# Performance work log

Hardware: AMD Instinct MI355X
Metric: run time of the kernel (lower is better)

## Reference

```python
import jax, jax.numpy as jnp
import numpy as np

B = 8            # graphs per batch
NP = 1000        # nodes per graph (fixed 1000x1000 connectivity)
N = B * NP       # total nodes
F = 1000         # node feature dim (== NP)
HC = 32          # hidden_channels
NL = 3           # num_layers (HC*NL == 96, the hard-coded bnh dim)
K = 5            # Chebyshev order
HID = 128        # mlp hidden
NC = 2           # num_classes
DEG = 10         # avg degree
E = N * DEG      # total edges
TRI = F * (F - 1) // 2   # 499500 strict-upper-triangle entries
EPS = 1e-5


def setup_inputs():
    ks = jax.random.split(jax.random.key(0), 16)
    x = jax.random.normal(ks[0], (N, F), jnp.float32)  # per-graph connectivity rows
    # block-structured edges: endpoints stay inside their own graph
    offs = jnp.repeat(jnp.arange(B, dtype=jnp.int32) * NP, NP * DEG)
    src = jax.random.randint(ks[1], (E,), 0, NP, jnp.int32) + offs
    dst = jax.random.randint(ks[2], (E,), 0, NP, jnp.int32) + offs
    edge_index = jnp.stack([src, dst])
    batch = jnp.repeat(jnp.arange(B, dtype=jnp.int32), NP)
    nrm = lambda k, shape, s=0.05: jax.random.normal(k, shape, jnp.float32) * s
    return dict(
        x=x, edge_index=edge_index, batch=batch,
        conv_w0=nrm(ks[3], (K, F, HC)), conv_b0=jnp.zeros((HC,), jnp.float32),
        conv_w1=nrm(ks[4], (K, HC, HC)), conv_b1=jnp.zeros((HC,), jnp.float32),
        conv_w2=nrm(ks[5], (K, HC, HC)), conv_b2=jnp.zeros((HC,), jnp.float32),
        bnh_g=jnp.ones((HC * NL,), jnp.float32), bnh_b=jnp.zeros((HC * NL,), jnp.float32),
        bn_g=jnp.ones((TRI,), jnp.float32), bn_b=jnp.zeros((TRI,), jnp.float32),
        mlp_w1=nrm(ks[6], (TRI, HID), 0.002), mlp_b1=jnp.zeros((HID,), jnp.float32),
        bn1_g=jnp.ones((HID,), jnp.float32), bn1_b=jnp.zeros((HID,), jnp.float32),
        mlp_w2=nrm(ks[7], (HID, HID // 2)), mlp_b2=jnp.zeros((HID // 2,), jnp.float32),
        bn2_g=jnp.ones((HID // 2,), jnp.float32), bn2_b=jnp.zeros((HID // 2,), jnp.float32),
        mlp_w3=nrm(ks[8], (HID // 2, HID // 2)), mlp_b3=jnp.zeros((HID // 2,), jnp.float32),
        bn3_g=jnp.ones((HID // 2,), jnp.float32), bn3_b=jnp.zeros((HID // 2,), jnp.float32),
        mlp_w4=nrm(ks[9], (HID // 2, NC)), mlp_b4=jnp.zeros((NC,), jnp.float32),
    )


def _bn(z, g, b):
    # BatchNorm1d in training mode (batch stats, biased var), eps=1e-5
    m = jnp.mean(z, axis=0)
    v = jnp.var(z, axis=0)
    return (z - m) * jax.lax.rsqrt(v + EPS) * g + b


def _cheb(z, src, dst, w, Ws, b):
    # PyG ChebConv with sym norm, lambda_max=2: L~ = -D^{-1/2} A D^{-1/2}
    prop = lambda t: jax.ops.segment_sum(w[:, None] * t[src], dst, num_segments=N)
    Tx0, out = z, z @ Ws[0]
    Tx1 = prop(z)
    out = out + Tx1 @ Ws[1]
    for k in range(2, Ws.shape[0]):
        Tx2 = 2.0 * prop(Tx1) - Tx0
        out = out + Tx2 @ Ws[k]
        Tx0, Tx1 = Tx1, Tx2
    return out + b


def reference(x, edge_index, batch, conv_w0, conv_b0, conv_w1, conv_b1, conv_w2, conv_b2,
              bnh_g, bnh_b, bn_g, bn_b, mlp_w1, mlp_b1, bn1_g, bn1_b,
              mlp_w2, mlp_b2, bn2_g, bn2_b, mlp_w3, mlp_b3, bn3_g, bn3_b, mlp_w4, mlp_b4):
    src, dst = edge_index[0], edge_index[1]
    # symmetric normalization weights (negated scaled Laplacian off-diagonal)
    deg = jax.ops.segment_sum(jnp.ones((E,), x.dtype), src, num_segments=N)
    dinv = jnp.where(deg > 0, deg ** -0.5, 0.0)
    w = -dinv[src] * dinv[dst]
    # node features replaced by tiled identity, as in the original forward
    xid = jnp.tile(jnp.eye(NP, dtype=x.dtype), (B, 1))  # [N, F]
    h1 = jnp.tanh(_cheb(xid, src, dst, w, conv_w0, conv_b0))
    h2 = jnp.tanh(_cheb(h1, src, dst, w, conv_w1, conv_b1))
    h3 = jnp.tanh(_cheb(h2, src, dst, w, conv_w2, conv_b2))
    # MeanAggregation per graph
    cnt = jax.ops.segment_sum(jnp.ones((N,), x.dtype), batch, num_segments=B)[:, None]
    pool = lambda h: jax.ops.segment_sum(h, batch, num_segments=B) / cnt
    emb = jnp.concatenate([pool(h1), pool(h2), pool(h3)], axis=1)  # [B, 96]
    hbn = _bn(emb, bnh_g, bnh_b)
    # static strict-upper-triangle gather (replaces per-graph triu().nonzero())
    rawx = x.reshape(B, F, F)
    iu0, iu1 = np.triu_indices(F, k=1)
    feats = rawx[:, iu0, iu1]                       # [B, 499500]
    fbn = _bn(feats, bn_g, bn_b)
    # MLP (dropout = identity / eval)
    a = jax.nn.relu(_bn(fbn @ mlp_w1 + mlp_b1, bn1_g, bn1_b))
    a = jax.nn.relu(_bn(a @ mlp_w2 + mlp_b2, bn2_g, bn2_b))
    a = jax.nn.relu(_bn(a @ mlp_w3 + mlp_b3, bn3_g, bn3_b))
    logits = a @ mlp_w4 + mlp_b4
    logp = jax.nn.log_softmax(logits, axis=1)
    return logp, hbn
```

## Files before the change

### kernel.cpp

```cpp
#include <hip/hip_runtime.h>

#define NN 8000
#define NPP 1000
#define FF 1000
#define HCC 32
#define KK 5
#define EE 80000
#define TRIN 499500
#define HID 128
#define EPSV 1e-5f
#define NREP 64

#define IDX_ACC  0
#define IDX_DEGI 65536
#define IDX_CNT  73536
#define IDX_FILL 81536
#define ZERO_N   89536
#define IDX_ROWS 89600
#define IDX_EPAK 97664
#define IDX_H1   257664
#define IDX_H2   513664
#define IDX_EMB  769664


__global__ void k_count(const int* __restrict__ src, const int* __restrict__ dst,
                        int* __restrict__ degi, int* __restrict__ cnt) {
  int e = blockIdx.x * blockDim.x + threadIdx.x;
  if (e >= EE) return;
  atomicAdd(&degi[src[e]], 1);
  atomicAdd(&cnt[dst[e]], 1);
}

__global__ void k_scan(const int* __restrict__ cnt, int* __restrict__ rows) {
  __shared__ int ssum[1024];
  int tid = threadIdx.x;
  int base = tid * 8;
  int loc[8];
  int s = 0;
#pragma unroll
  for (int q = 0; q < 8; ++q) {
    int idx = base + q;
    int v = (idx < NN) ? cnt[idx] : 0;
    loc[q] = s;
    s += v;
  }
  ssum[tid] = s;
  __syncthreads();
  for (int d = 1; d < 1024; d <<= 1) {
    int v = (tid >= d) ? ssum[tid - d] : 0;
    __syncthreads();
    ssum[tid] += v;
    __syncthreads();
  }
  int off = (tid == 0) ? 0 : ssum[tid - 1];
#pragma unroll
  for (int q = 0; q < 8; ++q) {
    int idx = base + q;
    if (idx < NN) rows[idx] = off + loc[q];
  }
  if (tid == 1023) rows[NN] = EE;
}

__global__ void k_fill(const int* __restrict__ src, const int* __restrict__ dst,
                       const int* __restrict__ degi, const int* __restrict__ rows,
                       int* __restrict__ fill, int2* __restrict__ epak) {
  int e = blockIdx.x * blockDim.x + threadIdx.x;
  if (e >= EE) return;
  int s = src[e], d = dst[e];
  int pos = rows[d] + atomicAdd(&fill[d], 1);
  int dd = degi[d];
  float w = -rsqrtf((float)degi[s]) * ((dd > 0) ? rsqrtf((float)dd) : 0.0f);
  int2 pk;
  pk.x = s % NPP;
  pk.y = __float_as_int(w);
  epak[pos] = pk;
}

__global__ void __launch_bounds__(1024, 4) k_layer(
    const float* __restrict__ cw, const float* __restrict__ bias,
    const float* __restrict__ hin, float* __restrict__ hout,
    const int* __restrict__ rows, const int2* __restrict__ epak,
    float* __restrict__ emb, int L) {
  __shared__ float ckl[KK][NPP];
  __shared__ float bcur[NPP];
  __shared__ float wcol[KK][HCC];
  __shared__ float part[32];
  const int t = threadIdx.x;
  const int g = blockIdx.x >> 5;
  const int c = blockIdx.x & 31;
  const bool act = t < NPP;
  if (hin == nullptr) {
    if (act) {
#pragma unroll
      for (int k = 0; k < KK; ++k)
        ckl[k][t] = cw[k * (FF * HCC) + t * HCC + c];
    }
  } else {
    if (t < KK * HCC) {
      int k = t >> 5, j = t & 31;
      wcol[k][j] = cw[k * (HCC * HCC) + j * HCC + c];
    }
    __syncthreads();
    if (act) {
      float hrow[HCC];
      const float* hp = hin + ((size_t)g * NPP + t) * HCC;
#pragma unroll
      for (int q = 0; q < HCC / 4; ++q) {
        float4 f = *(const float4*)(hp + q * 4);
        hrow[q * 4 + 0] = f.x; hrow[q * 4 + 1] = f.y;
        hrow[q * 4 + 2] = f.z; hrow[q * 4 + 3] = f.w;
      }
#pragma unroll
      for (int k = 0; k < KK; ++k) {
        float a = 0.0f;
#pragma unroll
        for (int j = 0; j < HCC; ++j) a += hrow[j] * wcol[k][j];
        ckl[k][t] = a;
      }
    }
  }
  __syncthreads();
  int r0 = 0, r1 = 0;
  if (act) {
    bcur[t] = ckl[4][t];
    r0 = rows[g * NPP + t];
    r1 = rows[g * NPP + t + 1];
  }
  float bprev = 0.0f;
  float v = 0.0f;
  __syncthreads();
#pragma unroll
  for (int step = 0; step < 4; ++step) {
    const float alpha = (step == 3) ? 1.0f : 2.0f;
    const int kidx = 3 - step;
    if (act) {
      float acc = 0.0f;
      for (int e = r0; e < r1; ++e) {
        int2 pk = epak[e];
        acc += __int_as_float(pk.y) * bcur[pk.x];
      }
      v = alpha * acc - bprev + ckl[kidx][t];
    }
    __syncthreads();
    if (act) {
      bprev = bcur[t];
      bcur[t] = v;
    }
    __syncthreads();
  }
  if (act) {
    float h = tanhf(v + bias[c]);
    if (hout) hout[((size_t)g * NPP + t) * HCC + c] = h;
    bcur[t] = h;
  }
  __syncthreads();
  if (t < 32) {
    float s = 0.0f;
    for (int i = t; i < NPP; i += 32) s += bcur[i];
    part[t] = s;
  }
  __syncthreads();
  if (t == 0) {
    float s = 0.0f;
#pragma unroll
    for (int q = 0; q < 32; ++q) s += part[q];
    emb[g * 96 + L * HCC + c] = s * (1.0f / (float)NPP);
  }
}


__device__ __forceinline__ int tri_S(int i) { return i * 999 - (i * (i - 1)) / 2; }

__global__ void __launch_bounds__(256) k_gemm1(const float* __restrict__ x,
                                               const float* __restrict__ bng,
                                               const float* __restrict__ bnb,
                                               const float* __restrict__ W1,
                                               float* __restrict__ accrep) {
  __shared__ float fbn_s[256][8];
  __shared__ float red[8][128];
  const int tid = threadIdx.x;
  const int c4 = (tid & 31) * 4;
  const int stripe = tid >> 5;
  const int j0 = blockIdx.x * 256;
  float acc[8][4];
#pragma unroll
  for (int b = 0; b < 8; ++b)
#pragma unroll
    for (int q = 0; q < 4; ++q) acc[b][q] = 0.0f;

  {
    const int j = j0 + tid;
    float vals[8];
    if (j < TRIN) {
      const float tt = 1999.0f;
      int i = (int)((tt - sqrtf(tt * tt - 8.0f * (float)j)) * 0.5f);
      i = max(0, min(i, 998));
      while (tri_S(i + 1) <= j) ++i;
      while (tri_S(i) > j) --i;
      int i1 = j - tri_S(i) + i + 1;
      size_t base = (size_t)i * FF + i1;
#pragma unroll
      for (int b = 0; b < 8; ++b) vals[b] = x[(size_t)b * (FF * NPP) + base];
      float m = 0.0f;
#pragma unroll
      for (int b = 0; b < 8; ++b) m += vals[b];
      m *= 0.125f;
      float va = 0.0f;
#pragma unroll
      for (int b = 0; b < 8; ++b) { float d = vals[b] - m; va += d * d; }
      va *= 0.125f;
      float sc = bng[j] * rsqrtf(va + EPSV);
      float tb = bnb[j] - m * sc;
#pragma unroll
      for (int b = 0; b < 8; ++b) vals[b] = sc * vals[b] + tb;
    } else {
#pragma unroll
      for (int b = 0; b < 8; ++b) vals[b] = 0.0f;
    }
    *(float4*)&fbn_s[tid][0] = make_float4(vals[0], vals[1], vals[2], vals[3]);
    *(float4*)&fbn_s[tid][4] = make_float4(vals[4], vals[5], vals[6], vals[7]);
  }
  __syncthreads();

  const int jbase = stripe * 32;
  const int jmax = min(32, TRIN - j0 - jbase);
  const float* wp = W1 + (size_t)(j0 + jbase) * HID + c4;
  if (jmax == 32) {
#pragma unroll 4
    for (int jj = 0; jj < 32; ++jj) {
      float4 w = *(const float4*)(wp + (size_t)jj * HID);
      float4 f0 = *(const float4*)&fbn_s[jbase + jj][0];
      float4 f1 = *(const float4*)&fbn_s[jbase + jj][4];
      float wv[4] = {w.x, w.y, w.z, w.w};
      float fv[8] = {f0.x, f0.y, f0.z, f0.w, f1.x, f1.y, f1.z, f1.w};
#pragma unroll
      for (int b = 0; b < 8; ++b)
#pragma unroll
        for (int q = 0; q < 4; ++q) acc[b][q] += fv[b] * wv[q];
    }
  } else {
    for (int jj = 0; jj < jmax; ++jj) {
      float4 w = *(const float4*)(wp + (size_t)jj * HID);
      float4 f0 = *(const float4*)&fbn_s[jbase + jj][0];
      float4 f1 = *(const float4*)&fbn_s[jbase + jj][4];
      float wv[4] = {w.x, w.y, w.z, w.w};
      float fv[8] = {f0.x, f0.y, f0.z, f0.w, f1.x, f1.y, f1.z, f1.w};
#pragma unroll
      for (int b = 0; b < 8; ++b)
#pragma unroll
        for (int q = 0; q < 4; ++q) acc[b][q] += fv[b] * wv[q];
    }
  }
#pragma unroll
  for (int b = 0; b < 8; ++b) {
    __syncthreads();
    red[stripe][c4 + 0] = acc[b][0];
    red[stripe][c4 + 1] = acc[b][1];
    red[stripe][c4 + 2] = acc[b][2];
    red[stripe][c4 + 3] = acc[b][3];
    __syncthreads();
    if (tid < 128) {
      float s = 0.0f;
#pragma unroll
      for (int q = 0; q < 8; ++q) s += red[q][tid];
      atomicAdd(&accrep[(blockIdx.x & (NREP - 1)) * 1024 + b * HID + tid], s);
    }
  }
}


__global__ void __launch_bounds__(1024) k_mlp(
    const float* __restrict__ accrep, const float* __restrict__ emb,
    const float* __restrict__ hg, const float* __restrict__ hb,
    const float* __restrict__ mb1,
    const float* __restrict__ g1, const float* __restrict__ be1,
    const float* __restrict__ W2, const float* __restrict__ mb2,
    const float* __restrict__ g2, const float* __restrict__ be2,
    const float* __restrict__ W3, const float* __restrict__ mb3,
    const float* __restrict__ g3, const float* __restrict__ be3,
    const float* __restrict__ W4, const float* __restrict__ mb4,
    float* __restrict__ out) {
  __shared__ float A[8][128];
  __shared__ float V[8][128];
  __shared__ float Bm[8][64];
  __shared__ float Cm[8][64];
  __shared__ float lg[8][2];
  const int tid = threadIdx.x;
  if (tid < 96) {
    float v[8];
    float m = 0.0f;
#pragma unroll
    for (int q = 0; q < 8; ++q) { v[q] = emb[q * 96 + tid]; m += v[q]; }
    m *= 0.125f;
    float va = 0.0f;
#pragma unroll
    for (int q = 0; q < 8; ++q) { float d = v[q] - m; va += d * d; }
    va *= 0.125f;
    float s = hg[tid] * rsqrtf(va + EPSV);
    float t = hb[tid] - m * s;
#pragma unroll
    for (int q = 0; q < 8; ++q) out[16 + q * 96 + tid] = s * v[q] + t;
  }
  {
    const int c = tid & 127;
    const int b = tid >> 7;
    float a = mb1[c];
    for (int rep = 0; rep < NREP; ++rep) a += accrep[rep * 1024 + tid];
    V[b][c] = a;
  }
  __syncthreads();
  {
    const int c = tid & 127;
    const int b = tid >> 7;
    float m = 0.0f;
#pragma unroll
    for (int q = 0; q < 8; ++q) m += V[q][c];
    m *= 0.125f;
    float va = 0.0f;
#pragma unroll
    for (int q = 0; q < 8; ++q) { float d = V[q][c] - m; va += d * d; }
    va *= 0.125f;
    float s = g1[c] * rsqrtf(va + EPSV);
    float t = be1[c] - m * s;
    float z = s * V[b][c] + t;
    A[b][c] = (z > 0.0f) ? z : 0.0f;
  }
  __syncthreads();
  if (tid < 512) {
    const int c = tid & 63;
    const int b = tid >> 6;
    float a = mb2[c];
    for (int j = 0; j < 128; ++j) a += A[b][j] * W2[j * 64 + c];
    V[b][c] = a;
  }
  __syncthreads();
  if (tid < 512) {
    const int c = tid & 63;
    const int b = tid >> 6;
    float m = 0.0f;
#pragma unroll
    for (int q = 0; q < 8; ++q) m += V[q][c];
    m *= 0.125f;
    float va = 0.0f;
#pragma unroll
    for (int q = 0; q < 8; ++q) { float d = V[q][c] - m; va += d * d; }
    va *= 0.125f;
    float s = g2[c] * rsqrtf(va + EPSV);
    float t = be2[c] - m * s;
    float z = s * V[b][c] + t;
    Bm[b][c] = (z > 0.0f) ? z : 0.0f;
  }
  __syncthreads();
  if (tid < 512) {
    const int c = tid & 63;
    const int b = tid >> 6;
    float a = mb3[c];
    for (int j = 0; j < 64; ++j) a += Bm[b][j] * W3[j * 64 + c];
    V[b][c] = a;
  }
  __syncthreads();
  if (tid < 512) {
    const int c = tid & 63;
    const int b = tid >> 6;
    float m = 0.0f;
#pragma unroll
    for (int q = 0; q < 8; ++q) m += V[q][c];
    m *= 0.125f;
    float va = 0.0f;
#pragma unroll
    for (int q = 0; q < 8; ++q) { float d = V[q][c] - m; va += d * d; }
    va *= 0.125f;
    float s = g3[c] * rsqrtf(va + EPSV);
    float t = be3[c] - m * s;
    float z = s * V[b][c] + t;
    Cm[b][c] = (z > 0.0f) ? z : 0.0f;
  }
  __syncthreads();
  if (tid < 16) {
    int b = tid >> 1, c = tid & 1;
    float a4 = mb4[c];
    for (int j = 0; j < 64; ++j) a4 += Cm[b][j] * W4[j * 2 + c];
    lg[b][c] = a4;
  }
  __syncthreads();
  if (tid < 8) {
    float l0 = lg[tid][0], l1 = lg[tid][1];
    float mm = fmaxf(l0, l1);
    float lse = mm + logf(expf(l0 - mm) + expf(l1 - mm));
    out[tid * 2 + 0] = l0 - lse;
    out[tid * 2 + 1] = l1 - lse;
  }
}


extern "C" void kernel_launch(void* const* d_in, const int* in_sizes, int n_in,
                              void* d_out, int out_size, void* d_ws, size_t ws_size,
                              hipStream_t stream) {
  const float* x = (const float*)d_in[0];
  const int* ei = (const int*)d_in[1];
  const int* src = ei;
  const int* dst = ei + EE;
  const float* cw0 = (const float*)d_in[3];
  const float* cb0 = (const float*)d_in[4];
  const float* cw1 = (const float*)d_in[5];
  const float* cb1 = (const float*)d_in[6];
  const float* cw2 = (const float*)d_in[7];
  const float* cb2 = (const float*)d_in[8];
  const float* bnhg = (const float*)d_in[9];
  const float* bnhb = (const float*)d_in[10];
  const float* bng = (const float*)d_in[11];
  const float* bnb = (const float*)d_in[12];
  const float* mw1 = (const float*)d_in[13];
  const float* mb1 = (const float*)d_in[14];
  const float* b1g = (const float*)d_in[15];
  const float* b1b = (const float*)d_in[16];
  const float* mw2 = (const float*)d_in[17];
  const float* mb2 = (const float*)d_in[18];
  const float* b2g = (const float*)d_in[19];
  const float* b2b = (const float*)d_in[20];
  const float* mw3 = (const float*)d_in[21];
  const float* mb3 = (const float*)d_in[22];
  const float* b3g = (const float*)d_in[23];
  const float* b3b = (const float*)d_in[24];
  const float* mw4 = (const float*)d_in[25];
  const float* mb4 = (const float*)d_in[26];

  float* ws = (float*)d_ws;
  int* wsi = (int*)d_ws;
  float* out = (float*)d_out;

  float* accrep = ws + IDX_ACC;
  int* degi = wsi + IDX_DEGI;
  int* cnt = wsi + IDX_CNT;
  int* fill = wsi + IDX_FILL;
  int* rows = wsi + IDX_ROWS;
  int2* epak = (int2*)(wsi + IDX_EPAK);
  float* h1 = ws + IDX_H1;
  float* h2 = ws + IDX_H2;
  float* emb = ws + IDX_EMB;

  hipMemsetAsync(wsi, 0, ZERO_N * sizeof(int), stream);

  k_gemm1<<<(TRIN + 255) / 256, 256, 0, stream>>>(x, bng, bnb, mw1, accrep);
  k_count<<<(EE + 255) / 256, 256, 0, stream>>>(src, dst, degi, cnt);
  k_scan<<<1, 1024, 0, stream>>>(cnt, rows);
  k_fill<<<(EE + 255) / 256, 256, 0, stream>>>(src, dst, degi, rows, fill, epak);
  k_layer<<<256, 1024, 0, stream>>>(cw0, cb0, nullptr, h1, rows, epak, emb, 0);
  k_layer<<<256, 1024, 0, stream>>>(cw1, cb1, h1, h2, rows, epak, emb, 1);
  k_layer<<<256, 1024, 0, stream>>>(cw2, cb2, h2, nullptr, rows, epak, emb, 2);
  k_mlp<<<1, 1024, 0, stream>>>(accrep, emb, bnhg, bnhb, mb1, b1g, b1b,
                                mw2, mb2, b2g, b2b, mw3, mb3, b3g, b3b,
                                mw4, mb4, out);
}
```

Before: 561.9 us.

## Replace CSR build with per-graph edge scatter using shared-memory atomics

New measurement: 623.1 us. 10.9% more time.

```diff
diff --git a/kernel.cpp b/kernel.cpp
--- a/kernel.cpp
+++ b/kernel.cpp
@@ -6,6 +6,8 @@
 #define HCC 32
 #define KK 5
 #define EE 80000
+#define EDGB 10000
+#define EPB 10240
 #define TRIN 499500
 #define HID 128
 #define EPSV 1e-5f
@@ -13,76 +15,41 @@
 
 #define IDX_ACC  0
 #define IDX_DEGI 65536
-#define IDX_CNT  73536
-#define IDX_FILL 81536
-#define ZERO_N   89536
-#define IDX_ROWS 89600
-#define IDX_EPAK 97664
-#define IDX_H1   257664
-#define IDX_H2   513664
-#define IDX_EMB  769664
-
-
-__global__ void k_count(const int* __restrict__ src, const int* __restrict__ dst,
-                        int* __restrict__ degi, int* __restrict__ cnt) {
+#define IDX_EPAK 73536
+#define ZERO_N   237376
+#define IDX_H1   237376
+#define IDX_H2   493376
+#define IDX_EMB  749376
+
+
+__global__ void k_count(const int* __restrict__ src, int* __restrict__ degi) {
   int e = blockIdx.x * blockDim.x + threadIdx.x;
   if (e >= EE) return;
   atomicAdd(&degi[src[e]], 1);
-  atomicAdd(&cnt[dst[e]], 1);
-}
-
-__global__ void k_scan(const int* __restrict__ cnt, int* __restrict__ rows) {
-  __shared__ int ssum[1024];
-  int tid = threadIdx.x;
-  int base = tid * 8;
-  int loc[8];
-  int s = 0;
-#pragma unroll
-  for (int q = 0; q < 8; ++q) {
-    int idx = base + q;
-    int v = (idx < NN) ? cnt[idx] : 0;
-    loc[q] = s;
-    s += v;
-  }
-  ssum[tid] = s;
-  __syncthreads();
-  for (int d = 1; d < 1024; d <<= 1) {
-    int v = (tid >= d) ? ssum[tid - d] : 0;
-    __syncthreads();
-    ssum[tid] += v;
-    __syncthreads();
-  }
-  int off = (tid == 0) ? 0 : ssum[tid - 1];
-#pragma unroll
-  for (int q = 0; q < 8; ++q) {
-    int idx = base + q;
-    if (idx < NN) rows[idx] = off + loc[q];
-  }
-  if (tid == 1023) rows[NN] = EE;
-}
-
-__global__ void k_fill(const int* __restrict__ src, const int* __restrict__ dst,
-                       const int* __restrict__ degi, const int* __restrict__ rows,
-                       int* __restrict__ fill, int2* __restrict__ epak) {
+}
+
+__global__ void k_pack(const int* __restrict__ src, const int* __restrict__ dst,
+                       const int* __restrict__ degi, int2* __restrict__ epak) {
   int e = blockIdx.x * blockDim.x + threadIdx.x;
   if (e >= EE) return;
   int s = src[e], d = dst[e];
-  int pos = rows[d] + atomicAdd(&fill[d], 1);
   int dd = degi[d];
   float w = -rsqrtf((float)degi[s]) * ((dd > 0) ? rsqrtf((float)dd) : 0.0f);
+  int g = e / EDGB;
   int2 pk;
-  pk.x = s % NPP;
+  pk.x = (s % NPP) | ((d % NPP) << 16);
   pk.y = __float_as_int(w);
-  epak[pos] = pk;
+  epak[e + g * (EPB - EDGB)] = pk;
 }
 
 __global__ void __launch_bounds__(1024, 4) k_layer(
     const float* __restrict__ cw, const float* __restrict__ bias,
     const float* __restrict__ hin, float* __restrict__ hout,
-    const int* __restrict__ rows, const int2* __restrict__ epak,
+    const int2* __restrict__ epak,
     float* __restrict__ emb, int L) {
   __shared__ float ckl[KK][NPP];
   __shared__ float bcur[NPP];
+  __shared__ float bnxt[NPP];
   __shared__ float wcol[KK][HCC];
   __shared__ float part[32];
   const int t = threadIdx.x;
@@ -120,31 +87,30 @@
     }
   }
   __syncthreads();
-  int r0 = 0, r1 = 0;
   if (act) {
-    bcur[t] = ckl[4][t];
-    r0 = rows[g * NPP + t];
-    r1 = rows[g * NPP + t + 1];
+    bcur[t] = ckl[KK - 1][t];
+    bnxt[t] = 0.0f;
   }
   float bprev = 0.0f;
   float v = 0.0f;
   __syncthreads();
+  const int2* ep = epak + (size_t)g * EPB;
 #pragma unroll
   for (int step = 0; step < 4; ++step) {
     const float alpha = (step == 3) ? 1.0f : 2.0f;
     const int kidx = 3 - step;
-    if (act) {
-      float acc = 0.0f;
-      for (int e = r0; e < r1; ++e) {
-        int2 pk = epak[e];
-        acc += __int_as_float(pk.y) * bcur[pk.x];
-      }
-      v = alpha * acc - bprev + ckl[kidx][t];
+#pragma unroll
+    for (int q = 0; q < EPB / 1024; ++q) {
+      int2 pk = ep[t + q * 1024];
+      float val = __int_as_float(pk.y) * bcur[pk.x & 0xffff];
+      atomicAdd(&bnxt[pk.x >> 16], val);
     }
     __syncthreads();
     if (act) {
+      v = alpha * bnxt[t] - bprev + ckl[kidx][t];
       bprev = bcur[t];
       bcur[t] = v;
+      bnxt[t] = 0.0f;
     }
     __syncthreads();
   }
@@ -305,6 +271,7 @@
     const int c = tid & 127;
     const int b = tid >> 7;
     float a = mb1[c];
+#pragma unroll 8
     for (int rep = 0; rep < NREP; ++rep) a += accrep[rep * 1024 + tid];
     V[b][c] = a;
   }
@@ -431,9 +398,6 @@
 
   float* accrep = ws + IDX_ACC;
   int* degi = wsi + IDX_DEGI;
-  int* cnt = wsi + IDX_CNT;
-  int* fill = wsi + IDX_FILL;
-  int* rows = wsi + IDX_ROWS;
   int2* epak = (int2*)(wsi + IDX_EPAK);
   float* h1 = ws + IDX_H1;
   float* h2 = ws + IDX_H2;
@@ -442,12 +406,11 @@
   hipMemsetAsync(wsi, 0, ZERO_N * sizeof(int), stream);
 
   k_gemm1<<<(TRIN + 255) / 256, 256, 0, stream>>>(x, bng, bnb, mw1, accrep);
-  k_count<<<(EE + 255) / 256, 256, 0, stream>>>(src, dst, degi, cnt);
-  k_scan<<<1, 1024, 0, stream>>>(cnt, rows);
-  k_fill<<<(EE + 255) / 256, 256, 0, stream>>>(src, dst, degi, rows, fill, epak);
-  k_layer<<<256, 1024, 0, stream>>>(cw0, cb0, nullptr, h1, rows, epak, emb, 0);
-  k_layer<<<256, 1024, 0, stream>>>(cw1, cb1, h1, h2, rows, epak, emb, 1);
-  k_layer<<<256, 1024, 0, stream>>>(cw2, cb2, h2, nullptr, rows, epak, emb, 2);
+  k_count<<<(EE + 255) / 256, 256, 0, stream>>>(src, degi);
+  k_pack<<<(EE + 255) / 256, 256, 0, stream>>>(src, dst, degi, epak);
+  k_layer<<<256, 1024, 0, stream>>>(cw0, cb0, nullptr, h1, epak, emb, 0);
+  k_layer<<<256, 1024, 0, stream>>>(cw1, cb1, h1, h2, epak, emb, 1);
+  k_layer<<<256, 1024, 0, stream>>>(cw2, cb2, h2, nullptr, epak, emb, 2);
   k_mlp<<<1, 1024, 0, stream>>>(accrep, emb, bnhg, bnhb, mb1, b1g, b1b,
                                 mw2, mb2, b2g, b2b, mw3, mb3, b3g, b3b,
                                 mw4, mb4, out);
```
